# Performance work log

Measured on AMD Instinct MI355X. Metric: run time of the kernel, lower is better.

## Reference

```python
import jax, jax.numpy as jnp
import numpy as np

PI = float(np.pi)


def _layernorm(x, g, b, eps=1e-5):
    mu = jnp.mean(x, axis=-1, keepdims=True)
    var = jnp.var(x, axis=-1, keepdims=True)
    return (x - mu) * jax.lax.rsqrt(var + eps) * g + b


def setup_inputs() -> dict:
    key = jax.random.key(0)
    B, L, D, P = 4, 2048, 256, 32
    ks = jax.random.split(key, 16)

    def lin_w(k, fi, fo):
        return (jax.random.normal(k, (fi, fo), dtype=jnp.float32) / np.sqrt(fi)).astype(jnp.float32)

    inp = {
        'x': jax.random.normal(ks[0], (B, L, D), dtype=jnp.float32),
        'pos_phases': jax.random.normal(ks[1], (L, P), dtype=jnp.float32) * PI,
        'w_mem1v': lin_w(ks[2], D, P), 'b_mem1v': jnp.zeros((P,), jnp.float32),
        'w_mem1o': lin_w(ks[3], P, D), 'b_mem1o': jnp.zeros((D,), jnp.float32),
        'w_off': lin_w(ks[4], D + P, P), 'b_off': jnp.zeros((P,), jnp.float32),
        'w_key': lin_w(ks[5], D, P), 'b_key': jnp.zeros((P,), jnp.float32),
        'w_val': lin_w(ks[6], D, D), 'b_val': jnp.zeros((D,), jnp.float32),
        'w_sk1': lin_w(ks[7], 2 * D, D), 'b_sk1': jnp.zeros((D,), jnp.float32),
        'w_sk2': lin_w(ks[8], D, P), 'b_sk2': jnp.zeros((P,), jnp.float32),
        'w_gate': lin_w(ks[9], D, 1), 'b_gate': jnp.zeros((1,), jnp.float32),
        'ln_g': jnp.ones((D,), jnp.float32), 'ln_b': jnp.zeros((D,), jnp.float32),
        'w_out': lin_w(ks[10], D, D), 'b_out': jnp.zeros((D,), jnp.float32),
    }
    return inp


def reference(x, pos_phases, w_mem1v, b_mem1v, w_mem1o, b_mem1o, w_off, b_off,
              w_key, b_key, w_val, b_val, w_sk1, b_sk1, w_sk2, b_sk2,
              w_gate, b_gate, ln_g, ln_b, w_out, b_out):
    B, L, D = x.shape
    P = pos_phases.shape[-1]

    pos_cos = jnp.cos(pos_phases)  # [L,P]
    pos_sin = jnp.sin(pos_phases)

    # Memory 1: flat [B,L,P] phasor cumulative memory
    v1 = x @ w_mem1v + b_mem1v                       # [B,L,P]
    mem1_cos = jnp.cumsum(pos_cos[None] * v1, axis=1)
    mem1_sin = jnp.cumsum(pos_sin[None] * v1, axis=1)

    offset_input = jnp.concatenate([x, jnp.broadcast_to(pos_phases[None], (B, L, P))], axis=-1)
    offset = jnp.tanh(offset_input @ w_off + b_off) * PI
    oc, os = jnp.cos(offset), jnp.sin(offset)
    query_cos = pos_cos[None] * oc - pos_sin[None] * os
    query_sin = pos_sin[None] * oc + pos_cos[None] * os
    pos_ret = (mem1_cos * query_cos + mem1_sin * query_sin) / np.sqrt(P)
    pos_out = pos_ret @ w_mem1o + b_mem1o            # [B,L,D]

    # Memory 2: full [B,L,P,D] phasor KV cumulative memory
    key_phases = jnp.tanh(x @ w_key + b_key) * PI    # [B,L,P]
    key_cos, key_sin = jnp.cos(key_phases), jnp.sin(key_phases)
    values = x @ w_val + b_val                       # [B,L,D]
    store_gate = jax.nn.sigmoid(x @ w_gate + b_gate) # [B,L,1]

    positions = jnp.arange(1, L + 1, dtype=x.dtype)[None, :, None]
    context_avg = jnp.cumsum(x, axis=1) / positions
    h = jax.nn.gelu(jnp.concatenate([x, context_avg], axis=-1) @ w_sk1 + b_sk1, approximate=False)
    storage_phases = jnp.tanh(h @ w_sk2 + b_sk2) * PI  # [B,L,P]

    gated_v = values * store_gate                    # [B,L,D]
    kv_mem_cos = jnp.cumsum(jnp.cos(storage_phases)[..., None] * gated_v[:, :, None, :], axis=1)  # [B,L,P,D]
    kv_mem_sin = jnp.cumsum(jnp.sin(storage_phases)[..., None] * gated_v[:, :, None, :], axis=1)

    gate_cumsum = jnp.clip(jnp.cumsum(store_gate, axis=1), 1.0, None)  # [B,L,1]
    kv_retrieved = jnp.einsum('blpd,blp->bld', kv_mem_cos, key_cos) + \
                   jnp.einsum('blpd,blp->bld', kv_mem_sin, key_sin)
    kv_retrieved = kv_retrieved / (jnp.sqrt(gate_cumsum) * np.sqrt(P))

    combined = pos_out + kv_retrieved
    return x + _layernorm(combined, ln_g, ln_b) @ w_out + b_out
```

## Files before the change

kernel.cpp:

```cpp
#include <hip/hip_runtime.h>
#include <hip/hip_bf16.h>

constexpr int B_ = 4;
constexpr int L_ = 2048;
constexpr int D_ = 256;
constexpr int P_ = 32;
constexpr int CL = 32;
constexpr int NC = L_ / CL;

#define PI_F 3.14159265358979323846f
#define INV_SQRT_P 0.17677669529663687f

typedef __attribute__((ext_vector_type(8))) short short8_t;
typedef __attribute__((ext_vector_type(4))) float floatx4;

static __device__ inline short f2bf(float f) {
  unsigned int u;
  __builtin_memcpy(&u, &f, 4);
  unsigned int r = (u + 0x7fffu + ((u >> 16) & 1u)) >> 16;
  return (short)r;
}
static __device__ inline float bf2f(short s) {
  unsigned int u = ((unsigned int)(unsigned short)s) << 16;
  float f;
  __builtin_memcpy(&f, &u, 4);
  return f;
}

__global__ void wprep(const float* __restrict__ x, const float* __restrict__ pos,
                      const float* __restrict__ w_val, const float* __restrict__ w_mem1v,
                      const float* __restrict__ w_off, const float* __restrict__ b_off,
                      const float* __restrict__ w_key, const float* __restrict__ w_gate,
                      const float* __restrict__ w_sk1, const float* __restrict__ w_out,
                      const float* __restrict__ w_sk2, const float* __restrict__ w_mem1o,
                      short* __restrict__ WA, short* __restrict__ W1,
                      short* __restrict__ WO, short* __restrict__ W2T,
                      short* __restrict__ W1OT,
                      short* __restrict__ xbf, float* __restrict__ poff) {
  int blk = blockIdx.x, tid = threadIdx.x;
  if (blk < 384) {
    int idx = blk * 256 + tid;
    int n = idx >> 8, k = idx & 255;
    float v;
    if (n < 256) v = w_val[k * 256 + n];
    else if (n < 288) v = w_mem1v[k * 32 + (n - 256)];
    else if (n < 320) v = w_off[k * 32 + (n - 288)];
    else if (n < 352) v = w_key[k * 32 + (n - 320)];
    else if (n == 352) v = w_gate[k];
    else v = 0.f;
    WA[idx] = f2bf(v);
  } else if (blk < 896) {
    int idx = (blk - 384) * 256 + tid;
    int n = idx >> 9, k = idx & 511;
    W1[idx] = f2bf(w_sk1[k * 256 + n]);
  } else if (blk < 1152) {
    int idx = (blk - 896) * 256 + tid;
    int n = idx >> 8, k = idx & 255;
    WO[idx] = f2bf(w_out[k * 256 + n]);
  } else if (blk < 1184) {
    int idx = (blk - 1152) * 256 + tid;
    int p = idx >> 8, k = idx & 255;
    W2T[idx] = f2bf(w_sk2[k * 32 + p]);
  } else if (blk < 1216) {
    int idx = (blk - 1184) * 256 + tid;
    int d = idx >> 5, p = idx & 31;
    W1OT[idx] = f2bf(w_mem1o[p * 256 + d]);
  } else if (blk < 3264) {
    int idx = ((blk - 1216) * 256 + tid) * 4;
    float4 v = *(const float4*)&x[idx];
    short4 o;
    o.x = f2bf(v.x); o.y = f2bf(v.y); o.z = f2bf(v.z); o.w = f2bf(v.w);
    *(short4*)&xbf[idx] = o;
  } else {
    int idx = (blk - 3264) * 256 + tid;
    int l = idx >> 5, p = idx & 31;
    float a = b_off[p];
    for (int j = 0; j < 32; ++j) a += pos[l * 32 + j] * w_off[(256 + j) * 32 + p];
    poff[idx] = a;
  }
}

template <int KTILES, int NBLK, int MODE>
__global__ __launch_bounds__(256) void gemm_k(const short* __restrict__ A0,
                                              const short* __restrict__ A1,
                                              const short* __restrict__ W,
                                              const float* __restrict__ bias,
                                              const float* __restrict__ xres,
                                              float* __restrict__ outf,
                                              short* __restrict__ outb) {
  __shared__ short As[64][136];
  __shared__ short Bs[64][136];
  int tid = threadIdx.x;
  int mg = blockIdx.x / NBLK, ng = blockIdx.x % NBLK;
  int tok0 = mg * 64, n0 = ng * 64;
  int lane = tid & 63, w = tid >> 6;
  int mw = (w & 1) * 32, nw = (w >> 1) * 32;
  floatx4 acc[2][2] = {{{0.f, 0.f, 0.f, 0.f}, {0.f, 0.f, 0.f, 0.f}},
                       {{0.f, 0.f, 0.f, 0.f}, {0.f, 0.f, 0.f, 0.f}}};
  int r2 = tid >> 4, c8 = tid & 15;
  int ml = lane & 15, kq = (lane >> 4) * 8;
  const int K = KTILES * 128;

  for (int kt = 0; kt < KTILES; ++kt) {
    const short* Asrc;
    int cb;
    if (KTILES == 4) {
      Asrc = (kt < 2) ? A0 : A1;
      cb = (kt & 1) * 128;
    } else {
      Asrc = A0;
      cb = kt * 128;
    }
#pragma unroll
    for (int pass = 0; pass < 4; ++pass) {
      int row = pass * 16 + r2;
      *(short8_t*)&As[row][c8 * 8] =
          *(const short8_t*)&Asrc[(tok0 + row) * 256 + cb + c8 * 8];
      *(short8_t*)&Bs[row][c8 * 8] =
          *(const short8_t*)&W[(n0 + row) * K + kt * 128 + c8 * 8];
    }
    __syncthreads();
#pragma unroll
    for (int s = 0; s < 4; ++s) {
      short8_t a0 = *(short8_t*)&As[mw + ml][s * 32 + kq];
      short8_t a1 = *(short8_t*)&As[mw + 16 + ml][s * 32 + kq];
      short8_t b0 = *(short8_t*)&Bs[nw + ml][s * 32 + kq];
      short8_t b1 = *(short8_t*)&Bs[nw + 16 + ml][s * 32 + kq];
      acc[0][0] = __builtin_amdgcn_mfma_f32_16x16x32_bf16(a0, b0, acc[0][0], 0, 0, 0);
      acc[0][1] = __builtin_amdgcn_mfma_f32_16x16x32_bf16(a0, b1, acc[0][1], 0, 0, 0);
      acc[1][0] = __builtin_amdgcn_mfma_f32_16x16x32_bf16(a1, b0, acc[1][0], 0, 0, 0);
      acc[1][1] = __builtin_amdgcn_mfma_f32_16x16x32_bf16(a1, b1, acc[1][1], 0, 0, 0);
    }
    __syncthreads();
  }
  int col = lane & 15, rq = (lane >> 4) * 4;
#pragma unroll
  for (int nt = 0; nt < 2; ++nt) {
    int n = n0 + nw + nt * 16 + col;
    float bv = (MODE == 0) ? 0.f : bias[n];
#pragma unroll
    for (int mt = 0; mt < 2; ++mt) {
#pragma unroll
      for (int rg = 0; rg < 4; ++rg) {
        int tok = tok0 + mw + mt * 16 + rq + rg;
        float v = acc[mt][nt][rg] + bv;
        if (MODE == 0) {
          outb[tok * 384 + n] = f2bf(v);
        } else if (MODE == 1) {
          float g = 0.5f * v * (1.f + erff(v * 0.70710678118654752f));
          outb[tok * 256 + n] = f2bf(g);
        } else {
          outf[tok * 256 + n] = xres[tok * 256 + n] + v;
        }
      }
    }
  }
}

__global__ void kernelA3(const short* __restrict__ Ybf, const float* __restrict__ pos,
                         const float* __restrict__ poff, const float* __restrict__ b_mem1v,
                         const float* __restrict__ b_key, const float* __restrict__ b_gate,
                         const float* __restrict__ b_val,
                         float* __restrict__ m1cT, float* __restrict__ m1sT,
                         float* __restrict__ qc, float* __restrict__ qs,
                         short* __restrict__ K2bf, short* __restrict__ gvT,
                         float* __restrict__ sg) {
  __shared__ float gsh[8];
  int tid = threadIdx.x;
  int tok0 = blockIdx.x * 8;
  int t = tid >> 5, p = tid & 31;
  int tok = tok0 + t, l = tok & (L_ - 1);
  int b = tok >> 11;
  float gate = 1.f / (1.f + expf(-(bf2f(Ybf[tok * 384 + 352]) + b_gate[0])));
  if (p == 0) {
    sg[tok] = gate;
    gsh[t] = gate;
  }
  float v1 = bf2f(Ybf[tok * 384 + 256 + p]) + b_mem1v[p];
  float ph = pos[l * 32 + p];
  float pc = cosf(ph), ps = sinf(ph);
  int idxT = (b * 32 + p) * L_ + l;
  m1cT[idxT] = pc * v1;
  m1sT[idxT] = ps * v1;
  float off = tanhf(bf2f(Ybf[tok * 384 + 288 + p]) + poff[l * 32 + p]) * PI_F;
  float oc = cosf(off), os = sinf(off);
  int idx = tok * 32 + p;
  qc[idx] = pc * oc - ps * os;
  qs[idx] = ps * oc + pc * os;
  float kp = tanhf(bf2f(Ybf[tok * 384 + 320 + p]) + b_key[p]) * PI_F;
  K2bf[tok * 64 + p] = f2bf(cosf(kp));
  K2bf[tok * 64 + 32 + p] = f2bf(sinf(kp));
  __syncthreads();
  {
    int l0 = tok0 & (L_ - 1);
    int bc = (tok0 >> 11) * NC + (l0 >> 5);
    int tl0 = l0 & 31;
    short sv[8];
#pragma unroll
    for (int tt = 0; tt < 8; ++tt)
      sv[tt] = f2bf((bf2f(Ybf[(tok0 + tt) * 384 + tid]) + b_val[tid]) * gsh[tt]);
    *(short8_t*)&gvT[(bc * 256 + tid) * 32 + tl0] = *(short8_t*)sv;
  }
}

__global__ void scan_all(float* __restrict__ m1cT, float* __restrict__ m1sT,
                         float* __restrict__ sg, const float* __restrict__ x,
                         float* __restrict__ ctxsum) {
  int blk = blockIdx.x;
  int tid = threadIdx.x;
  if (blk >= 260) {
    int c2 = blk - 260;
    int b = c2 >> 6, ch = c2 & 63;
    int xb = (b * L_ + ch * 32) * 256 + tid;
    float s = 0.f;
#pragma unroll 8
    for (int i = 0; i < 32; ++i) s += x[xb + i * 256];
    ctxsum[c2 * 256 + tid] = s;
    return;
  }
  int lane = tid & 63, wid = tid >> 6;
  __shared__ float wsum[4];
  float carry = 0.f;
  float* arr;
  int base;
  if (blk < 256) {
    arr = (blk < 128) ? m1cT : m1sT;
    base = (blk & 127) * L_;
  } else {
    arr = sg;
    base = (blk - 256) * L_;
  }
  for (int t0 = 0; t0 < L_; t0 += 256) {
    int l = t0 + tid;
    float v = arr[base + l];
#pragma unroll
    for (int off = 1; off < 64; off <<= 1) {
      float n = __shfl_up(v, off, 64);
      if (lane >= off) v += n;
    }
    if (lane == 63) wsum[wid] = v;
    __syncthreads();
    float add = carry;
    for (int w = 0; w < wid; ++w) add += wsum[w];
    arr[base + l] = v + add;
    carry += wsum[0] + wsum[1] + wsum[2] + wsum[3];
    __syncthreads();
  }
}

__global__ void kernelCtx(const float* __restrict__ x, const float* __restrict__ ctxsum,
                          short* __restrict__ ctxbf) {
  int c2 = blockIdx.x;
  int b = c2 >> 6, ch = c2 & 63;
  int tid = threadIdx.x;
  float run = 0.f;
  int sb = b * 64 * 256 + tid;
  for (int c = 0; c < ch; ++c) run += ctxsum[sb + c * 256];
  int xb = (b * L_ + ch * 32) * 256 + tid;
#pragma unroll 8
  for (int i = 0; i < 32; ++i) {
    run += x[xb + i * 256];
    int l = ch * 32 + i;
    ctxbf[xb + i * 256] = f2bf(run / (float)(l + 1));
  }
}

__global__ __launch_bounds__(256) void kernelCD(const short* __restrict__ hs,
                                                const short* __restrict__ W2T,
                                                const float* __restrict__ b_sk2,
                                                const short* __restrict__ gvT,
                                                short* __restrict__ SPbf,
                                                short* __restrict__ UT) {
  __shared__ __align__(16) short SPL[2][64][40];
  int tid = threadIdx.x;
  int tok0 = blockIdx.x * 64;
  int lane = tid & 63, w = tid >> 6;
  int ml = lane & 15, quad = lane >> 4, kq = quad * 8;
  int m0 = w * 16;
  floatx4 pacc[2] = {};
#pragma unroll
  for (int s = 0; s < 8; ++s) {
    short8_t a = *(const short8_t*)&hs[(tok0 + m0 + ml) * 256 + s * 32 + kq];
    short8_t b0 = *(const short8_t*)&W2T[ml * 256 + s * 32 + kq];
    short8_t b1 = *(const short8_t*)&W2T[(16 + ml) * 256 + s * 32 + kq];
    pacc[0] = __builtin_amdgcn_mfma_f32_16x16x32_bf16(a, b0, pacc[0], 0, 0, 0);
    pacc[1] = __builtin_amdgcn_mfma_f32_16x16x32_bf16(a, b1, pacc[1], 0, 0, 0);
  }
  int cl = w >> 1;
#pragma unroll
  for (int nt = 0; nt < 2; ++nt) {
    int p = nt * 16 + ml;
    float bs = b_sk2[p];
#pragma unroll
    for (int r = 0; r < 4; ++r) {
      int tok = tok0 + m0 + quad * 4 + r;
      float sp = tanhf(pacc[nt][r] + bs) * PI_F;
      short c = f2bf(cosf(sp)), s = f2bf(sinf(sp));
      int tl = (w & 1) * 16 + quad * 4 + r;
      SPL[cl][p][tl] = c;
      SPL[cl][32 + p][tl] = s;
      SPbf[tok * 64 + p] = c;
      SPbf[tok * 64 + 32 + p] = s;
    }
  }
  __syncthreads();
  int c2 = w & 1, dbase = (w >> 1) * 128;
  int bc = blockIdx.x * 2 + c2;
  short8_t a[4];
#pragma unroll
  for (int mt = 0; mt < 4; ++mt) a[mt] = *(short8_t*)&SPL[c2][mt * 16 + ml][kq];
#pragma unroll
  for (int dp = 0; dp < 2; ++dp) {
    floatx4 acc[4][4] = {};
#pragma unroll
    for (int nt = 0; nt < 4; ++nt) {
      short8_t b = *(const short8_t*)&gvT[(bc * 256 + dbase + dp * 64 + nt * 16 + ml) * 32 + kq];
#pragma unroll
      for (int mt = 0; mt < 4; ++mt)
        acc[mt][nt] = __builtin_amdgcn_mfma_f32_16x16x32_bf16(a[mt], b, acc[mt][nt], 0, 0, 0);
    }
#pragma unroll
    for (int mt = 0; mt < 4; ++mt)
#pragma unroll
      for (int nt = 0; nt < 4; ++nt)
#pragma unroll
        for (int r = 0; r < 4; ++r) {
          int q = mt * 16 + quad * 4 + r;
          int d = dbase + dp * 64 + nt * 16 + ml;
          UT[(bc * 256 + d) * 64 + q] = f2bf(acc[mt][nt][r]);
        }
  }
}

__global__ void kernelE(short* __restrict__ UT) {
  int tid = blockIdx.x * 256 + threadIdx.x;
  int q = tid & 63;
  int d = (tid >> 6) & 255;
  int b = tid >> 14;
  int base = ((b * NC) * 256 + d) * 64 + q;
  const int cs = 256 * 64;
  float run = 0.f;
  for (int c0 = 0; c0 < NC; c0 += 8) {
    short v[8];
#pragma unroll
    for (int j = 0; j < 8; ++j) v[j] = UT[base + (c0 + j) * cs];
#pragma unroll
    for (int j = 0; j < 8; ++j) {
      UT[base + (c0 + j) * cs] = f2bf(run);
      run += bf2f(v[j]);
    }
  }
}

__global__ __launch_bounds__(256) void kernelFG(const short* __restrict__ UT,
                                                const short* __restrict__ SPbf,
                                                const short* __restrict__ K2bf,
                                                const short* __restrict__ gvT,
                                                const float* __restrict__ sgc,
                                                const float* __restrict__ m1cT,
                                                const float* __restrict__ m1sT,
                                                const float* __restrict__ qc,
                                                const float* __restrict__ qs,
                                                const short* __restrict__ W1OT,
                                                const float* __restrict__ b_mem1o,
                                                const float* __restrict__ ln_g,
                                                const float* __restrict__ ln_b,
                                                short* __restrict__ cbn) {
  __shared__ __align__(16) short SL[32][40];
  __shared__ __align__(16) short PR[32][40];
  __shared__ float CMB[32][260];
  __shared__ float scl[32], mu_s[32], rs_s[32];
  int tid = threadIdx.x;
  int bc = blockIdx.x;
  int lbase = bc * CL;
  int bb = bc >> 6, lloc = (bc & 63) * 32;
  if (tid < 32) scl[tid] = rsqrtf(fmaxf(sgc[lbase + tid], 1.f)) * INV_SQRT_P;
  for (int it = 0; it < 4; ++it) {
    int i = it * 256 + tid;
    int p = i >> 5, t = i & 31;
    int gT = (bb * 32 + p) * L_ + lloc + t;
    int g = (lbase + t) * 32 + p;
    PR[t][p] = f2bf((m1cT[gT] * qc[g] + m1sT[gT] * qs[g]) * INV_SQRT_P);
  }
  int lane = tid & 63, w = tid >> 6;
  int ml = lane & 15, quad = lane >> 4, kq = quad * 8;
  floatx4 acc[2][4] = {};
  short8_t ka0 = *(const short8_t*)&K2bf[(lbase + ml) * 64 + kq];
  short8_t ka1 = *(const short8_t*)&K2bf[(lbase + 16 + ml) * 64 + kq];
  short8_t kb0 = *(const short8_t*)&K2bf[(lbase + ml) * 64 + 32 + kq];
  short8_t kb1 = *(const short8_t*)&K2bf[(lbase + 16 + ml) * 64 + 32 + kq];
#pragma unroll
  for (int nt = 0; nt < 4; ++nt) {
    short8_t b = *(const short8_t*)&UT[(bc * 256 + w * 64 + nt * 16 + ml) * 64 + kq];
    acc[0][nt] = __builtin_amdgcn_mfma_f32_16x16x32_bf16(ka0, b, acc[0][nt], 0, 0, 0);
    acc[1][nt] = __builtin_amdgcn_mfma_f32_16x16x32_bf16(ka1, b, acc[1][nt], 0, 0, 0);
  }
  if (w == 0) {
    floatx4 sacc[2][2] = {};
#pragma unroll
    for (int ks2 = 0; ks2 < 2; ++ks2) {
      short8_t a0 = (ks2 == 0) ? ka0 : kb0;
      short8_t a1 = (ks2 == 0) ? ka1 : kb1;
      short8_t b0 = *(const short8_t*)&SPbf[(lbase + ml) * 64 + ks2 * 32 + kq];
      short8_t b1 = *(const short8_t*)&SPbf[(lbase + 16 + ml) * 64 + ks2 * 32 + kq];
      sacc[0][0] = __builtin_amdgcn_mfma_f32_16x16x32_bf16(a0, b0, sacc[0][0], 0, 0, 0);
      sacc[0][1] = __builtin_amdgcn_mfma_f32_16x16x32_bf16(a0, b1, sacc[0][1], 0, 0, 0);
      sacc[1][0] = __builtin_amdgcn_mfma_f32_16x16x32_bf16(a1, b0, sacc[1][0], 0, 0, 0);
      sacc[1][1] = __builtin_amdgcn_mfma_f32_16x16x32_bf16(a1, b1, sacc[1][1], 0, 0, 0);
    }
#pragma unroll
    for (int mt = 0; mt < 2; ++mt)
#pragma unroll
      for (int nt = 0; nt < 2; ++nt)
#pragma unroll
        for (int r = 0; r < 4; ++r) {
          int trow = mt * 16 + quad * 4 + r;
          int scol = nt * 16 + ml;
          float v = (scol <= trow) ? sacc[mt][nt][r] : 0.f;
          SL[trow][scol] = f2bf(v);
        }
  }
  __syncthreads();
#pragma unroll
  for (int nt = 0; nt < 4; ++nt) {
    short8_t b = *(const short8_t*)&UT[(bc * 256 + w * 64 + nt * 16 + ml) * 64 + 32 + kq];
    acc[0][nt] = __builtin_amdgcn_mfma_f32_16x16x32_bf16(kb0, b, acc[0][nt], 0, 0, 0);
    acc[1][nt] = __builtin_amdgcn_mfma_f32_16x16x32_bf16(kb1, b, acc[1][nt], 0, 0, 0);
  }
  {
    short8_t a0 = *(short8_t*)&SL[ml][kq];
    short8_t a1 = *(short8_t*)&SL[16 + ml][kq];
#pragma unroll
    for (int nt = 0; nt < 4; ++nt) {
      short8_t b = *(const short8_t*)&gvT[(bc * 256 + w * 64 + nt * 16 + ml) * 32 + kq];
      acc[0][nt] = __builtin_amdgcn_mfma_f32_16x16x32_bf16(a0, b, acc[0][nt], 0, 0, 0);
      acc[1][nt] = __builtin_amdgcn_mfma_f32_16x16x32_bf16(a1, b, acc[1][nt], 0, 0, 0);
    }
  }
  floatx4 macc[2][4] = {};
  {
    short8_t a0 = *(short8_t*)&PR[ml][kq];
    short8_t a1 = *(short8_t*)&PR[16 + ml][kq];
#pragma unroll
    for (int nt = 0; nt < 4; ++nt) {
      short8_t b = *(const short8_t*)&W1OT[(w * 64 + nt * 16 + ml) * 32 + kq];
      macc[0][nt] = __builtin_amdgcn_mfma_f32_16x16x32_bf16(a0, b, macc[0][nt], 0, 0, 0);
      macc[1][nt] = __builtin_amdgcn_mfma_f32_16x16x32_bf16(a1, b, macc[1][nt], 0, 0, 0);
    }
  }
#pragma unroll
  for (int mt = 0; mt < 2; ++mt)
#pragma unroll
    for (int nt = 0; nt < 4; ++nt) {
      int d = w * 64 + nt * 16 + ml;
      float bm = b_mem1o[d];
#pragma unroll
      for (int r = 0; r < 4; ++r) {
        int t = mt * 16 + quad * 4 + r;
        CMB[t][d] = acc[mt][nt][r] * scl[t] + macc[mt][nt][r] + bm;
      }
    }
  __syncthreads();
  {
    int t = tid >> 3, g = tid & 7;
    float s = 0.f, s2 = 0.f;
#pragma unroll
    for (int j = 0; j < 32; ++j) {
      float v = CMB[t][g + j * 8];
      s += v;
      s2 += v * v;
    }
#pragma unroll
    for (int m = 1; m < 8; m <<= 1) {
      s += __shfl_xor(s, m, 64);
      s2 += __shfl_xor(s2, m, 64);
    }
    if (g == 0) {
      float mu = s / (float)D_;
      float var = s2 / (float)D_ - mu * mu;
      mu_s[t] = mu;
      rs_s[t] = rsqrtf(var + 1e-5f);
    }
  }
  __syncthreads();
  {
    float lg = ln_g[tid], lb = ln_b[tid];
#pragma unroll
    for (int t = 0; t < 32; ++t)
      cbn[(lbase + t) * 256 + tid] = f2bf((CMB[t][tid] - mu_s[t]) * rs_s[t] * lg + lb);
  }
}

extern "C" void kernel_launch(void* const* d_in, const int* in_sizes, int n_in,
                              void* d_out, int out_size, void* d_ws, size_t ws_size,
                              hipStream_t stream) {
  const float* x = (const float*)d_in[0];
  const float* pos = (const float*)d_in[1];
  const float* w_mem1v = (const float*)d_in[2];
  const float* b_mem1v = (const float*)d_in[3];
  const float* w_mem1o = (const float*)d_in[4];
  const float* b_mem1o = (const float*)d_in[5];
  const float* w_off = (const float*)d_in[6];
  const float* b_off = (const float*)d_in[7];
  const float* w_key = (const float*)d_in[8];
  const float* b_key = (const float*)d_in[9];
  const float* w_val = (const float*)d_in[10];
  const float* b_val = (const float*)d_in[11];
  const float* w_sk1 = (const float*)d_in[12];
  const float* b_sk1 = (const float*)d_in[13];
  const float* w_sk2 = (const float*)d_in[14];
  const float* b_sk2 = (const float*)d_in[15];
  const float* w_gate = (const float*)d_in[16];
  const float* b_gate = (const float*)d_in[17];
  const float* ln_g = (const float*)d_in[18];
  const float* ln_b = (const float*)d_in[19];
  const float* w_out = (const float*)d_in[20];
  const float* b_out = (const float*)d_in[21];
  float* out = (float*)d_out;
  float* ws = (float*)d_ws;

  const int BLP = B_ * L_ * P_;
  const int BLD = B_ * L_ * D_;
  float* m1cT = ws;
  float* m1sT = m1cT + BLP;
  float* qc = m1sT + BLP;
  float* qs = qc + BLP;
  float* sg = qs + BLP;
  float* poff = sg + B_ * L_;
  float* ctxsum = poff + L_ * P_;
  short* Ybf = (short*)(ctxsum + B_ * 64 * 256);
  short* UT = Ybf;
  short* xbf = UT + (size_t)B_ * NC * 256 * 64;
  short* cbn = xbf;
  short* ctxbf = xbf + BLD;
  short* hs = ctxbf + BLD;
  short* gvT = hs + BLD;
  short* K2bf = gvT + BLD;
  short* SPbf = K2bf + B_ * L_ * 64;
  short* WA = SPbf + B_ * L_ * 64;
  short* W1 = WA + 384 * 256;
  short* WO = W1 + 256 * 512;
  short* W2T = WO + 256 * 256;
  short* W1OT = W2T + 32 * 256;

  wprep<<<3520, 256, 0, stream>>>(x, pos, w_val, w_mem1v, w_off, b_off, w_key, w_gate,
                                  w_sk1, w_out, w_sk2, w_mem1o, WA, W1, WO, W2T, W1OT,
                                  xbf, poff);
  gemm_k<2, 6, 0><<<128 * 6, 256, 0, stream>>>(xbf, nullptr, WA, nullptr, nullptr, nullptr, Ybf);
  kernelA3<<<(B_ * L_) / 8, 256, 0, stream>>>(Ybf, pos, poff, b_mem1v, b_key, b_gate, b_val,
                                              m1cT, m1sT, qc, qs, K2bf, gvT, sg);
  scan_all<<<516, 256, 0, stream>>>(m1cT, m1sT, sg, x, ctxsum);
  kernelCtx<<<256, 256, 0, stream>>>(x, ctxsum, ctxbf);
  gemm_k<4, 4, 1><<<128 * 4, 256, 0, stream>>>(xbf, ctxbf, W1, b_sk1, nullptr, nullptr, hs);
  kernelCD<<<(B_ * L_) / 64, 256, 0, stream>>>(hs, W2T, b_sk2, gvT, SPbf, UT);
  kernelE<<<256, 256, 0, stream>>>(UT);
  kernelFG<<<B_ * NC, 256, 0, stream>>>(UT, SPbf, K2bf, gvT, sg, m1cT, m1sT, qc, qs,
                                        W1OT, b_mem1o, ln_g, ln_b, cbn);
  gemm_k<2, 4, 2><<<128 * 4, 256, 0, stream>>>(cbn, nullptr, WO, b_out, x, out, nullptr);
}
```

Baseline: 187.7 us.

## Fuse projection GEMM with pointwise phase epilogue and merge context-sum kernels

Measured after the change: 186.9 us. About the same (-0.4%).

```diff
diff --git a/kernel.cpp b/kernel.cpp
--- a/kernel.cpp
+++ b/kernel.cpp
@@ -36,7 +36,8 @@
                       short* __restrict__ WA, short* __restrict__ W1,
                       short* __restrict__ WO, short* __restrict__ W2T,
                       short* __restrict__ W1OT,
-                      short* __restrict__ xbf, float* __restrict__ poff) {
+                      short* __restrict__ xbf, float* __restrict__ poff,
+                      float* __restrict__ ctxsum) {
   int blk = blockIdx.x, tid = threadIdx.x;
   if (blk < 384) {
     int idx = blk * 256 + tid;
@@ -71,12 +72,20 @@
     short4 o;
     o.x = f2bf(v.x); o.y = f2bf(v.y); o.z = f2bf(v.z); o.w = f2bf(v.w);
     *(short4*)&xbf[idx] = o;
-  } else {
+  } else if (blk < 3520) {
     int idx = (blk - 3264) * 256 + tid;
     int l = idx >> 5, p = idx & 31;
     float a = b_off[p];
     for (int j = 0; j < 32; ++j) a += pos[l * 32 + j] * w_off[(256 + j) * 32 + p];
     poff[idx] = a;
+  } else {
+    int c2 = blk - 3520;
+    int b = c2 >> 6, ch = c2 & 63;
+    int xb = (b * L_ + ch * 32) * 256 + tid;
+    float s = 0.f;
+#pragma unroll 8
+    for (int i = 0; i < 32; ++i) s += x[xb + i * 256];
+    ctxsum[c2 * 256 + tid] = s;
   }
 }
 
@@ -157,65 +166,121 @@
   }
 }
 
-__global__ void kernelA3(const short* __restrict__ Ybf, const float* __restrict__ pos,
-                         const float* __restrict__ poff, const float* __restrict__ b_mem1v,
-                         const float* __restrict__ b_key, const float* __restrict__ b_gate,
-                         const float* __restrict__ b_val,
-                         float* __restrict__ m1cT, float* __restrict__ m1sT,
-                         float* __restrict__ qc, float* __restrict__ qs,
-                         short* __restrict__ K2bf, short* __restrict__ gvT,
-                         float* __restrict__ sg) {
-  __shared__ float gsh[8];
+__global__ __launch_bounds__(384) void gemmA3(const short* __restrict__ xbf,
+                                              const short* __restrict__ WA,
+                                              const float* __restrict__ pos,
+                                              const float* __restrict__ poff,
+                                              const float* __restrict__ b_mem1v,
+                                              const float* __restrict__ b_key,
+                                              const float* __restrict__ b_gate,
+                                              const float* __restrict__ b_val,
+                                              float* __restrict__ m1cT,
+                                              float* __restrict__ m1sT,
+                                              float* __restrict__ qc,
+                                              float* __restrict__ qs,
+                                              short* __restrict__ K2bf,
+                                              short* __restrict__ gvT,
+                                              float* __restrict__ sg) {
+  __shared__ float YL[32][132];
+  __shared__ float gsh[32];
   int tid = threadIdx.x;
-  int tok0 = blockIdx.x * 8;
-  int t = tid >> 5, p = tid & 31;
-  int tok = tok0 + t, l = tok & (L_ - 1);
-  int b = tok >> 11;
-  float gate = 1.f / (1.f + expf(-(bf2f(Ybf[tok * 384 + 352]) + b_gate[0])));
-  if (p == 0) {
-    sg[tok] = gate;
-    gsh[t] = gate;
-  }
-  float v1 = bf2f(Ybf[tok * 384 + 256 + p]) + b_mem1v[p];
-  float ph = pos[l * 32 + p];
-  float pc = cosf(ph), ps = sinf(ph);
-  int idxT = (b * 32 + p) * L_ + l;
-  m1cT[idxT] = pc * v1;
-  m1sT[idxT] = ps * v1;
-  float off = tanhf(bf2f(Ybf[tok * 384 + 288 + p]) + poff[l * 32 + p]) * PI_F;
-  float oc = cosf(off), os = sinf(off);
-  int idx = tok * 32 + p;
-  qc[idx] = pc * oc - ps * os;
-  qs[idx] = ps * oc + pc * os;
-  float kp = tanhf(bf2f(Ybf[tok * 384 + 320 + p]) + b_key[p]) * PI_F;
-  K2bf[tok * 64 + p] = f2bf(cosf(kp));
-  K2bf[tok * 64 + 32 + p] = f2bf(sinf(kp));
+  int lane = tid & 63, w = tid >> 6;
+  int ml = lane & 15, quad = lane >> 4, kq = quad * 8;
+  int bc = blockIdx.x;
+  int tok0 = bc * 32;
+  floatx4 acc[2][4] = {};
+  const short* A0p = &xbf[(tok0 + ml) * 256 + kq];
+  const short* A1p = &xbf[(tok0 + 16 + ml) * 256 + kq];
+  const short* Bp = &WA[(w * 64 + ml) * 256 + kq];
+#pragma unroll
+  for (int ks = 0; ks < 8; ++ks) {
+    short8_t a0 = *(const short8_t*)(A0p + ks * 32);
+    short8_t a1 = *(const short8_t*)(A1p + ks * 32);
+#pragma unroll
+    for (int nt = 0; nt < 4; ++nt) {
+      short8_t b = *(const short8_t*)(Bp + nt * 16 * 256 + ks * 32);
+      acc[0][nt] = __builtin_amdgcn_mfma_f32_16x16x32_bf16(a0, b, acc[0][nt], 0, 0, 0);
+      acc[1][nt] = __builtin_amdgcn_mfma_f32_16x16x32_bf16(a1, b, acc[1][nt], 0, 0, 0);
+    }
+  }
+  if (w >= 4) {
+#pragma unroll
+    for (int mt = 0; mt < 2; ++mt)
+#pragma unroll
+      for (int nt = 0; nt < 4; ++nt) {
+        int col = (w - 4) * 64 + nt * 16 + ml;
+#pragma unroll
+        for (int r = 0; r < 4; ++r)
+          YL[mt * 16 + quad * 4 + r][col] = acc[mt][nt][r];
+      }
+  }
   __syncthreads();
-  {
-    int l0 = tok0 & (L_ - 1);
-    int bc = (tok0 >> 11) * NC + (l0 >> 5);
-    int tl0 = l0 & 31;
-    short sv[8];
-#pragma unroll
-    for (int tt = 0; tt < 8; ++tt)
-      sv[tt] = f2bf((bf2f(Ybf[(tok0 + tt) * 384 + tid]) + b_val[tid]) * gsh[tt]);
-    *(short8_t*)&gvT[(bc * 256 + tid) * 32 + tl0] = *(short8_t*)sv;
+  if (tid < 256) {
+#pragma unroll
+    for (int it = 0; it < 4; ++it) {
+      int idx = it * 256 + tid;
+      int t = idx >> 5, p = idx & 31;
+      int tok = tok0 + t, l = tok & (L_ - 1);
+      int b = tok >> 11;
+      float v1 = YL[t][p] + b_mem1v[p];
+      float ph = pos[l * 32 + p];
+      float pc = cosf(ph), ps = sinf(ph);
+      int idxT = (b * 32 + p) * L_ + l;
+      m1cT[idxT] = pc * v1;
+      m1sT[idxT] = ps * v1;
+      float off = tanhf(YL[t][32 + p] + poff[l * 32 + p]) * PI_F;
+      float oc = cosf(off), os = sinf(off);
+      int gidx = tok * 32 + p;
+      qc[gidx] = pc * oc - ps * os;
+      qs[gidx] = ps * oc + pc * os;
+      float kp = tanhf(YL[t][64 + p] + b_key[p]) * PI_F;
+      K2bf[tok * 64 + p] = f2bf(cosf(kp));
+      K2bf[tok * 64 + 32 + p] = f2bf(sinf(kp));
+      if (p == 0) {
+        float g = 1.f / (1.f + expf(-(YL[t][96] + b_gate[0])));
+        sg[tok] = g;
+        gsh[t] = g;
+      }
+    }
+  }
+  __syncthreads();
+  if (w < 4) {
+#pragma unroll
+    for (int nt = 0; nt < 4; ++nt) {
+      int d = w * 64 + nt * 16 + ml;
+      float bv = b_val[d];
+#pragma unroll
+      for (int mt = 0; mt < 2; ++mt) {
+        int t0 = mt * 16 + quad * 4;
+        short4 o;
+        o.x = f2bf((acc[mt][nt][0] + bv) * gsh[t0 + 0]);
+        o.y = f2bf((acc[mt][nt][1] + bv) * gsh[t0 + 1]);
+        o.z = f2bf((acc[mt][nt][2] + bv) * gsh[t0 + 2]);
+        o.w = f2bf((acc[mt][nt][3] + bv) * gsh[t0 + 3]);
+        *(short4*)&gvT[(bc * 256 + d) * 32 + t0] = o;
+      }
+    }
   }
 }
 
 __global__ void scan_all(float* __restrict__ m1cT, float* __restrict__ m1sT,
                          float* __restrict__ sg, const float* __restrict__ x,
-                         float* __restrict__ ctxsum) {
+                         const float* __restrict__ ctxsum, short* __restrict__ ctxbf) {
   int blk = blockIdx.x;
   int tid = threadIdx.x;
   if (blk >= 260) {
     int c2 = blk - 260;
     int b = c2 >> 6, ch = c2 & 63;
+    float run = 0.f;
+    int sb = b * 64 * 256 + tid;
+    for (int c = 0; c < ch; ++c) run += ctxsum[sb + c * 256];
     int xb = (b * L_ + ch * 32) * 256 + tid;
-    float s = 0.f;
 #pragma unroll 8
-    for (int i = 0; i < 32; ++i) s += x[xb + i * 256];
-    ctxsum[c2 * 256 + tid] = s;
+    for (int i = 0; i < 32; ++i) {
+      run += x[xb + i * 256];
+      int l = ch * 32 + i;
+      ctxbf[xb + i * 256] = f2bf(run / (float)(l + 1));
+    }
     return;
   }
   int lane = tid & 63, wid = tid >> 6;
@@ -245,23 +310,6 @@
     arr[base + l] = v + add;
     carry += wsum[0] + wsum[1] + wsum[2] + wsum[3];
     __syncthreads();
-  }
-}
-
-__global__ void kernelCtx(const float* __restrict__ x, const float* __restrict__ ctxsum,
-                          short* __restrict__ ctxbf) {
-  int c2 = blockIdx.x;
-  int b = c2 >> 6, ch = c2 & 63;
-  int tid = threadIdx.x;
-  float run = 0.f;
-  int sb = b * 64 * 256 + tid;
-  for (int c = 0; c < ch; ++c) run += ctxsum[sb + c * 256];
-  int xb = (b * L_ + ch * 32) * 256 + tid;
-#pragma unroll 8
-  for (int i = 0; i < 32; ++i) {
-    run += x[xb + i * 256];
-    int l = ch * 32 + i;
-    ctxbf[xb + i * 256] = f2bf(run / (float)(l + 1));
   }
 }
 
@@ -528,8 +576,7 @@
   float* sg = qs + BLP;
   float* poff = sg + B_ * L_;
   float* ctxsum = poff + L_ * P_;
-  short* Ybf = (short*)(ctxsum + B_ * 64 * 256);
-  short* UT = Ybf;
+  short* UT = (short*)(ctxsum + B_ * 64 * 256);
   short* xbf = UT + (size_t)B_ * NC * 256 * 64;
   short* cbn = xbf;
   short* ctxbf = xbf + BLD;
@@ -543,14 +590,12 @@
   short* W2T = WO + 256 * 256;
   short* W1OT = W2T + 32 * 256;
 
-  wprep<<<3520, 256, 0, stream>>>(x, pos, w_val, w_mem1v, w_off, b_off, w_key, w_gate,
+  wprep<<<3776, 256, 0, stream>>>(x, pos, w_val, w_mem1v, w_off, b_off, w_key, w_gate,
                                   w_sk1, w_out, w_sk2, w_mem1o, WA, W1, WO, W2T, W1OT,
-                                  xbf, poff);
-  gemm_k<2, 6, 0><<<128 * 6, 256, 0, stream>>>(xbf, nullptr, WA, nullptr, nullptr, nullptr, Ybf);
-  kernelA3<<<(B_ * L_) / 8, 256, 0, stream>>>(Ybf, pos, poff, b_mem1v, b_key, b_gate, b_val,
-                                              m1cT, m1sT, qc, qs, K2bf, gvT, sg);
-  scan_all<<<516, 256, 0, stream>>>(m1cT, m1sT, sg, x, ctxsum);
-  kernelCtx<<<256, 256, 0, stream>>>(x, ctxsum, ctxbf);
+                                  xbf, poff, ctxsum);
+  gemmA3<<<256, 384, 0, stream>>>(xbf, WA, pos, poff, b_mem1v, b_key, b_gate, b_val,
+                                  m1cT, m1sT, qc, qs, K2bf, gvT, sg);
+  scan_all<<<516, 256, 0, stream>>>(m1cT, m1sT, sg, x, ctxsum, ctxbf);
   gemm_k<4, 4, 1><<<128 * 4, 256, 0, stream>>>(xbf, ctxbf, W1, b_sk1, nullptr, nullptr, hs);
   kernelCD<<<(B_ * L_) / 64, 256, 0, stream>>>(hs, W2T, b_sk2, gvT, SPbf, UT);
   kernelE<<<256, 256, 0, stream>>>(UT);
```
